# Kernel optimization log

Measured on AMD Instinct MI355X. Metric: run time of the kernel, lower is better.

## Reference

```python
import jax, jax.numpy as jnp
import numpy as np

N_NODES = 50000
N_EDGES = 800000
NUM_MOL = 2000
MSG_PASSES = 4


def setup_inputs() -> dict:
    key = jax.random.key(0)
    ks = jax.random.split(key, 16)
    x = jax.random.randint(ks[0], (N_NODES,), 0, 119)
    edge_attr = jax.random.randint(ks[1], (N_EDGES,), 0, 4)
    edge_index = jax.random.randint(ks[2], (2, N_EDGES), 0, N_NODES)
    batch = jnp.sort(jax.random.randint(ks[3], (N_NODES,), 0, NUM_MOL))
    f32 = jnp.float32
    return {
        "x": x,
        "edge_attr": edge_attr,
        "edge_index": edge_index,
        "batch": batch,
        "atom_table": jax.random.normal(ks[4], (119, 128), f32) * 0.1,
        "bond_table": jax.random.normal(ks[5], (4, 64), f32) * 0.1,
        "Wi": jax.random.normal(ks[6], (192, 128), f32) * 0.05,
        "bi": jax.random.normal(ks[7], (128,), f32) * 0.01,
        "Wu1": jax.random.normal(ks[8], (320, 128), f32) * 0.05,
        "bu1": jax.random.normal(ks[9], (128,), f32) * 0.01,
        "Wu2": jax.random.normal(ks[10], (128, 128), f32) * 0.05,
        "bu2": jax.random.normal(ks[11], (128,), f32) * 0.01,
        "Wr1": jax.random.normal(ks[12], (128, 512), f32) * 0.05,
        "br1": jax.random.normal(ks[13], (512,), f32) * 0.01,
        "Wr2": jax.random.normal(ks[14], (512, 1), f32) * 0.05,
        "br2": jax.random.normal(ks[15], (1,), f32) * 0.01,
    }


def reference(x, edge_attr, edge_index, batch,
              atom_table, bond_table, Wi, bi, Wu1, bu1, Wu2, bu2,
              Wr1, br1, Wr2, br2):
    atom = atom_table[x]                      # [N, atom_emb]
    bond = bond_table[edge_attr]              # [E, bond_emb]
    src, dst = edge_index[0], edge_index[1]
    a_src = atom[src]                         # [E, atom_emb]
    ab = jnp.concatenate([a_src, bond], axis=1)  # [E, atom_emb+bond_emb]
    msg = jax.nn.relu(ab @ Wi + bi)           # [E, msg_dim]
    for _ in range(MSG_PASSES):
        agg = jax.ops.segment_sum(msg, dst, num_segments=N_NODES)  # [N, msg_dim]
        upd_in = jnp.concatenate([ab, agg[src]], axis=1)           # [E, 320]
        h = jax.nn.relu(upd_in @ Wu1 + bu1)
        msg = jax.nn.relu(h @ Wu2 + bu2)
    node_state = jax.ops.segment_sum(msg, dst, num_segments=N_NODES)
    mol_state = jax.ops.segment_sum(node_state, batch, num_segments=NUM_MOL)
    out = jax.nn.relu(mol_state @ Wr1 + br1) @ Wr2 + br2  # [NUM_MOL, 1]
    return jnp.squeeze(out, axis=-1)
```

## Files before the change

### kernel.cpp

```cpp
#include <hip/hip_runtime.h>
#include <hip/hip_bf16.h>

#define N_NODES 50000
#define N_EDGES 800000
#define NUM_MOL 2000

typedef __attribute__((ext_vector_type(8))) short short8;
typedef __attribute__((ext_vector_type(4))) float f32x4;

union bfbits { __hip_bfloat16 b; short s; };

__global__ void k_tables(const float* __restrict__ atom_table,
                         const float* __restrict__ bond_table,
                         const float* __restrict__ Wi,
                         const float* __restrict__ bi,
                         const float* __restrict__ Wu1,
                         const float* __restrict__ bu1,
                         float* __restrict__ T1, float* __restrict__ U1,
                         float* __restrict__ T2c, float* __restrict__ U2c) {
  int b = blockIdx.x;
  int c = threadIdx.x;
  if (b < 119) {
    float t = 0.f, u = 0.f;
    for (int k = 0; k < 128; k++) {
      float a = atom_table[b * 128 + k];
      t += a * Wi[k * 128 + c];
      u += a * Wu1[k * 128 + c];
    }
    T1[b * 128 + c] = t;
    U1[b * 128 + c] = u;
  } else {
    int a = b - 119;
    float t = bi[c], u = bu1[c];
    for (int k = 0; k < 64; k++) {
      float bv = bond_table[a * 64 + k];
      t += bv * Wi[(128 + k) * 128 + c];
      u += bv * Wu1[(128 + k) * 128 + c];
    }
    T2c[a * 128 + c] = t;
    U2c[a * 128 + c] = u;
  }
}

__global__ void k_prep(const float* __restrict__ T1, const float* __restrict__ T2c,
                       const float* __restrict__ Wu2, const float* __restrict__ Wu1,
                       float* __restrict__ TT,
                       short* __restrict__ Wt, short* __restrict__ Wlo,
                       short* __restrict__ W1t, short* __restrict__ W1lo) {
  int b = blockIdx.x;
  int k = threadIdx.x;
  if (b < 476) {
    float v = T1[(b >> 2) * 128 + k] + T2c[(b & 3) * 128 + k];
    TT[b * 128 + k] = v > 0.f ? v : 0.f;
  } else if (b < 604) {
    int n = b - 476;
    float w = Wu2[k * 128 + n];
    bfbits hi; hi.b = __float2bfloat16(w);
    float hf = __bfloat162float(hi.b);
    bfbits lo; lo.b = __float2bfloat16(w - hf);
    Wt[n * 128 + k] = hi.s;
    Wlo[n * 128 + k] = lo.s;
  } else {
    int n = b - 604;
    float w = Wu1[(192 + k) * 128 + n];
    bfbits hi; hi.b = __float2bfloat16(w);
    float hf = __bfloat162float(hi.b);
    bfbits lo; lo.b = __float2bfloat16(w - hf);
    W1t[n * 128 + k] = hi.s;
    W1lo[n * 128 + k] = lo.s;
  }
}

__global__ void k_u1x(const int* __restrict__ x, const float* __restrict__ U1,
                      float* __restrict__ D_) {
  int n = blockIdx.x * 4 + (threadIdx.x >> 6);
  int lane = threadIdx.x & 63;
  int xn = x[n];
  float2 v = *(const float2*)&U1[xn * 128 + lane * 2];
  *(float2*)&D_[n * 128 + lane * 2] = v;
}

__global__ void k_fillb(const int* __restrict__ eidx, const int* __restrict__ attr,
                        const int* __restrict__ x,
                        int* __restrict__ cnt, int* __restrict__ csr1) {
  int e = blockIdx.x * 256 + threadIdx.x;
  int d = eidx[N_EDGES + e];
  int s = eidx[e];
  int a = attr[e];
  int pos = atomicAdd(&cnt[d], 1);
  if (pos < 64) {
    int packed = (s * 4 + a) | ((x[s] * 4 + a) << 18);
    csr1[d * 64 + pos] = packed;
  }
}

__global__ void k_molptr(const int* __restrict__ batch, int* __restrict__ molptr) {
  int m = blockIdx.x * 256 + threadIdx.x;
  if (m > NUM_MOL) return;
  int lo = 0, hi = N_NODES;
  while (lo < hi) {
    int mid = (lo + hi) >> 1;
    if (batch[mid] < m) lo = mid + 1; else hi = mid;
  }
  molptr[m] = lo;
}

__global__ void k_gather0(const int* __restrict__ cnt, const int* __restrict__ csr1,
                          const float* __restrict__ TT, float* __restrict__ A_) {
  int n = blockIdx.x * 4 + (threadIdx.x >> 6);
  int lane = threadIdx.x & 63;
  int g = lane >> 5;
  int p = lane & 31;
  int beg = n * 64;
  int end = beg + cnt[n];
  float s0 = 0.f, s1 = 0.f, s2 = 0.f, s3 = 0.f;
  int i = beg;
  for (; i + 7 < end; i += 8) {
    int iA = ((unsigned)csr1[i + g]) >> 18;
    int iB = ((unsigned)csr1[i + 2 + g]) >> 18;
    int iC = ((unsigned)csr1[i + 4 + g]) >> 18;
    int iD = ((unsigned)csr1[i + 6 + g]) >> 18;
    float4 va = *(const float4*)&TT[iA * 128 + p * 4];
    float4 vb = *(const float4*)&TT[iB * 128 + p * 4];
    float4 vc = *(const float4*)&TT[iC * 128 + p * 4];
    float4 vd = *(const float4*)&TT[iD * 128 + p * 4];
    s0 += (va.x + vb.x) + (vc.x + vd.x);
    s1 += (va.y + vb.y) + (vc.y + vd.y);
    s2 += (va.z + vb.z) + (vc.z + vd.z);
    s3 += (va.w + vb.w) + (vc.w + vd.w);
  }
  for (; i + 3 < end; i += 4) {
    int iA = ((unsigned)csr1[i + g]) >> 18;
    int iB = ((unsigned)csr1[i + 2 + g]) >> 18;
    float4 va = *(const float4*)&TT[iA * 128 + p * 4];
    float4 vb = *(const float4*)&TT[iB * 128 + p * 4];
    s0 += va.x + vb.x; s1 += va.y + vb.y;
    s2 += va.z + vb.z; s3 += va.w + vb.w;
  }
  for (; i < end; i += 2) {
    if (i + g < end) {
      int idx = ((unsigned)csr1[i + g]) >> 18;
      float4 v = *(const float4*)&TT[idx * 128 + p * 4];
      s0 += v.x; s1 += v.y; s2 += v.z; s3 += v.w;
    }
  }
  s0 += __shfl_xor(s0, 32, 64);
  s1 += __shfl_xor(s1, 32, 64);
  s2 += __shfl_xor(s2, 32, 64);
  s3 += __shfl_xor(s3, 32, 64);
  float2 o;
  o.x = (g == 0) ? s0 : s2;
  o.y = (g == 0) ? s1 : s3;
  *(float2*)&A_[n * 128 + p * 4 + g * 2] = o;
}

__global__ void k_gather(const int* __restrict__ cnt, const int* __restrict__ csr1,
                         const __hip_bfloat16* __restrict__ M, float* __restrict__ A_) {
  int n = blockIdx.x * 4 + (threadIdx.x >> 6);
  int lane = threadIdx.x & 63;
  int g = lane >> 4;
  int p = lane & 15;
  int beg = n * 64;
  int end = beg + cnt[n];
  float s[8];
#pragma unroll
  for (int j = 0; j < 8; j++) s[j] = 0.f;
  const short* Ms = (const short*)M;
  int i = beg;
  for (; i + 15 < end; i += 16) {
    int iA = csr1[i + g] & 0x3FFFF;
    int iB = csr1[i + 4 + g] & 0x3FFFF;
    int iC = csr1[i + 8 + g] & 0x3FFFF;
    int iD = csr1[i + 12 + g] & 0x3FFFF;
    short8 va = *(const short8*)&Ms[iA * 128 + p * 8];
    short8 vb = *(const short8*)&Ms[iB * 128 + p * 8];
    short8 vc = *(const short8*)&Ms[iC * 128 + p * 8];
    short8 vd = *(const short8*)&Ms[iD * 128 + p * 8];
#pragma unroll
    for (int j = 0; j < 4; j++) {
      float2 fa = __bfloat1622float2(*(const __hip_bfloat162*)&((const short*)&va)[j * 2]);
      float2 fb = __bfloat1622float2(*(const __hip_bfloat162*)&((const short*)&vb)[j * 2]);
      float2 fc = __bfloat1622float2(*(const __hip_bfloat162*)&((const short*)&vc)[j * 2]);
      float2 fd = __bfloat1622float2(*(const __hip_bfloat162*)&((const short*)&vd)[j * 2]);
      s[j * 2] += (fa.x + fb.x) + (fc.x + fd.x);
      s[j * 2 + 1] += (fa.y + fb.y) + (fc.y + fd.y);
    }
  }
  for (; i + 7 < end; i += 8) {
    int iA = csr1[i + g] & 0x3FFFF;
    int iB = csr1[i + 4 + g] & 0x3FFFF;
    short8 va = *(const short8*)&Ms[iA * 128 + p * 8];
    short8 vb = *(const short8*)&Ms[iB * 128 + p * 8];
#pragma unroll
    for (int j = 0; j < 4; j++) {
      float2 fa = __bfloat1622float2(*(const __hip_bfloat162*)&((const short*)&va)[j * 2]);
      float2 fb = __bfloat1622float2(*(const __hip_bfloat162*)&((const short*)&vb)[j * 2]);
      s[j * 2] += fa.x + fb.x;
      s[j * 2 + 1] += fa.y + fb.y;
    }
  }
  for (; i < end; i += 4) {
    if (i + g < end) {
      int idx = csr1[i + g] & 0x3FFFF;
      short8 va = *(const short8*)&Ms[idx * 128 + p * 8];
#pragma unroll
      for (int j = 0; j < 4; j++) {
        float2 fa = __bfloat1622float2(*(const __hip_bfloat162*)&((const short*)&va)[j * 2]);
        s[j * 2] += fa.x;
        s[j * 2 + 1] += fa.y;
      }
    }
  }
#pragma unroll
  for (int j = 0; j < 8; j++) s[j] += __shfl_xor(s[j], 16, 64);
#pragma unroll
  for (int j = 0; j < 8; j++) s[j] += __shfl_xor(s[j], 32, 64);
  float2 o;
  o.x = s[g * 2];
  o.y = s[g * 2 + 1];
  *(float2*)&A_[n * 128 + p * 8 + g * 2] = o;
}

__global__ __launch_bounds__(256, 2) void k_mm1m(const float* __restrict__ A_,
                                                 const short* __restrict__ W1t,
                                                 const short* __restrict__ W1lo,
                                                 const float* __restrict__ D_,
                                                 float* __restrict__ B2_) {
  __shared__ float mbuf[4][16][68];
  int t = threadIdx.x;
  int lane = t & 63;
  int m = lane & 15;
  int quad = lane >> 4;
  int wslot = t >> 6;
  int w0 = blockIdx.x * 4 + wslot;
  int h = w0 & 1;

  short8 whi[4][4], wlo[4][4];
#pragma unroll
  for (int kc = 0; kc < 4; kc++)
#pragma unroll
    for (int nt = 0; nt < 4; nt++) {
      int n = h * 64 + nt * 16 + m;
      whi[kc][nt] = *(const short8*)&W1t[n * 128 + kc * 32 + quad * 8];
      wlo[kc][nt] = *(const short8*)&W1lo[n * 128 + kc * 32 + quad * 8];
    }

  for (int tid = w0; tid < 6250; tid += 4096) {
    int s = tid >> 1;
    int row = s * 16 + m;
    f32x4 acc[4];
#pragma unroll
    for (int nt = 0; nt < 4; nt++) acc[nt] = (f32x4){0.f, 0.f, 0.f, 0.f};

#pragma unroll
    for (int kc = 0; kc < 4; kc++) {
      int k0 = kc * 32 + quad * 8;
      short8 ahi, alo;
      {
        float av[8];
        *(float4*)&av[0] = *(const float4*)&A_[row * 128 + k0];
        *(float4*)&av[4] = *(const float4*)&A_[row * 128 + k0 + 4];
#pragma unroll
        for (int j = 0; j < 8; j++) {
          float hv = av[j];
          bfbits hi; hi.b = __float2bfloat16(hv);
          float hf = __bfloat162float(hi.b);
          bfbits lo; lo.b = __float2bfloat16(hv - hf);
          ahi[j] = hi.s;
          alo[j] = lo.s;
        }
      }
#pragma unroll
      for (int nt = 0; nt < 4; nt++) {
        acc[nt] = __builtin_amdgcn_mfma_f32_16x16x32_bf16(ahi, whi[kc][nt], acc[nt], 0, 0, 0);
        acc[nt] = __builtin_amdgcn_mfma_f32_16x16x32_bf16(alo, whi[kc][nt], acc[nt], 0, 0, 0);
        acc[nt] = __builtin_amdgcn_mfma_f32_16x16x32_bf16(ahi, wlo[kc][nt], acc[nt], 0, 0, 0);
      }
    }

#pragma unroll
    for (int nt = 0; nt < 4; nt++)
#pragma unroll
      for (int r = 0; r < 4; r++)
        mbuf[wslot][quad * 4 + r][nt * 16 + m] = acc[nt][r];
#pragma unroll
    for (int p = 0; p < 4; p++) {
      int c = p * 64 + lane;
      int rr = c >> 4;
      int qf = c & 15;
      int n = s * 16 + rr;
      float4 v = *(const float4*)&mbuf[wslot][rr][qf * 4];
      float4 d = *(const float4*)&D_[n * 128 + h * 64 + qf * 4];
      v.x += d.x; v.y += d.y; v.z += d.z; v.w += d.w;
      *(float4*)&B2_[n * 128 + h * 64 + qf * 4] = v;
    }
  }
}

__global__ __launch_bounds__(256, 2) void k_mm2(const float* __restrict__ B2_,
                                                const float* __restrict__ U2c,
                                                const short* __restrict__ Wt,
                                                const short* __restrict__ Wlo,
                                                const float* __restrict__ bu2,
                                                __hip_bfloat16* __restrict__ M) {
  __shared__ short mbuf[4][16][68];
  int t = threadIdx.x;
  int lane = t & 63;
  int m = lane & 15;
  int quad = lane >> 4;
  int wslot = t >> 6;
  int w0 = blockIdx.x * 4 + wslot;
  int h = w0 & 1;

  short8 whi[4][4], wlo[4][4];
#pragma unroll
  for (int kc = 0; kc < 4; kc++)
#pragma unroll
    for (int nt = 0; nt < 4; nt++) {
      int n = h * 64 + nt * 16 + m;
      whi[kc][nt] = *(const short8*)&Wt[n * 128 + kc * 32 + quad * 8];
      wlo[kc][nt] = *(const short8*)&Wlo[n * 128 + kc * 32 + quad * 8];
    }
  float bias[4];
#pragma unroll
  for (int nt = 0; nt < 4; nt++) bias[nt] = bu2[h * 64 + nt * 16 + m];

  for (int tid = w0; tid < 25000; tid += 4096) {
    int s = tid >> 1;
    int node = s * 4 + (m >> 2);
    int attr = m & 3;
    f32x4 acc[4];
#pragma unroll
    for (int nt = 0; nt < 4; nt++) acc[nt] = (f32x4){0.f, 0.f, 0.f, 0.f};

#pragma unroll
    for (int kc = 0; kc < 4; kc++) {
      int k0 = kc * 32 + quad * 8;
      short8 ahi, alo;
      {
        float bba[8], u2a[8];
        *(float4*)&bba[0] = *(const float4*)&B2_[node * 128 + k0];
        *(float4*)&bba[4] = *(const float4*)&B2_[node * 128 + k0 + 4];
        *(float4*)&u2a[0] = *(const float4*)&U2c[attr * 128 + k0];
        *(float4*)&u2a[4] = *(const float4*)&U2c[attr * 128 + k0 + 4];
#pragma unroll
        for (int j = 0; j < 8; j++) {
          float hv = bba[j] + u2a[j];
          hv = hv > 0.f ? hv : 0.f;
          bfbits hi; hi.b = __float2bfloat16(hv);
          float hf = __bfloat162float(hi.b);
          bfbits lo; lo.b = __float2bfloat16(hv - hf);
          ahi[j] = hi.s;
          alo[j] = lo.s;
        }
      }
#pragma unroll
      for (int nt = 0; nt < 4; nt++) {
        acc[nt] = __builtin_amdgcn_mfma_f32_16x16x32_bf16(ahi, whi[kc][nt], acc[nt], 0, 0, 0);
        acc[nt] = __builtin_amdgcn_mfma_f32_16x16x32_bf16(alo, whi[kc][nt], acc[nt], 0, 0, 0);
        acc[nt] = __builtin_amdgcn_mfma_f32_16x16x32_bf16(ahi, wlo[kc][nt], acc[nt], 0, 0, 0);
      }
    }

#pragma unroll
    for (int nt = 0; nt < 4; nt++) {
#pragma unroll
      for (int r = 0; r < 4; r++) {
        float v = acc[nt][r] + bias[nt];
        v = v > 0.f ? v : 0.f;
        bfbits o; o.b = __float2bfloat16(v);
        mbuf[wslot][quad * 4 + r][nt * 16 + m] = o.s;
      }
    }
    {
      int rr = lane >> 2;
      int qq = lane & 3;
      short8 v = *(const short8*)&mbuf[wslot][rr][qq * 8];
      *(short8*)((short*)M + (s * 16 + rr) * 128 + h * 64 + qq * 8) = v;
      short8 v2 = *(const short8*)&mbuf[wslot][rr][(qq + 4) * 8];
      *(short8*)((short*)M + (s * 16 + rr) * 128 + h * 64 + (qq + 4) * 8) = v2;
    }
  }
}

__global__ void k_molgather(const float* __restrict__ A_, const int* __restrict__ molptr,
                            float* __restrict__ mol) {
  int m = blockIdx.x * 4 + (threadIdx.x >> 6);
  int lane = threadIdx.x & 63;
  int beg = molptr[m], end = molptr[m + 1];
  float ax = 0.f, ay = 0.f;
  int n = beg;
  for (; n + 1 < end; n += 2) {
    float2 v0 = *(const float2*)&A_[n * 128 + lane * 2];
    float2 v1 = *(const float2*)&A_[(n + 1) * 128 + lane * 2];
    ax += v0.x + v1.x;
    ay += v0.y + v1.y;
  }
  if (n < end) {
    float2 v0 = *(const float2*)&A_[n * 128 + lane * 2];
    ax += v0.x;
    ay += v0.y;
  }
  float2 o; o.x = ax; o.y = ay;
  *(float2*)&mol[m * 128 + lane * 2] = o;
}

__global__ __launch_bounds__(256) void k_readout(const float* __restrict__ mol,
                                                 const float* __restrict__ Wr1,
                                                 const float* __restrict__ br1,
                                                 const float* __restrict__ Wr2,
                                                 const float* __restrict__ br2,
                                                 float* __restrict__ out) {
  int m = blockIdx.x;
  __shared__ float ms[128];
  __shared__ float red[256];
  int t = threadIdx.x;
  if (t < 128) ms[t] = mol[m * 128 + t];
  __syncthreads();
  float part = 0.f;
#pragma unroll
  for (int jj = 0; jj < 2; jj++) {
    int j = t + jj * 256;
    float acc = br1[j];
#pragma unroll
    for (int k = 0; k < 128; k += 4) {
      float4 m4 = *(const float4*)&ms[k];
      acc += m4.x * Wr1[k * 512 + j] + m4.y * Wr1[(k + 1) * 512 + j] +
             m4.z * Wr1[(k + 2) * 512 + j] + m4.w * Wr1[(k + 3) * 512 + j];
    }
    acc = acc > 0.f ? acc : 0.f;
    part += acc * Wr2[j];
  }
  red[t] = part;
  __syncthreads();
  for (int s = 128; s > 0; s >>= 1) {
    if (t < s) red[t] += red[t + s];
    __syncthreads();
  }
  if (t == 0) out[m] = red[0] + br2[0];
}

extern "C" void kernel_launch(void* const* d_in, const int* in_sizes, int n_in,
                              void* d_out, int out_size, void* d_ws, size_t ws_size,
                              hipStream_t stream) {
  const int* x        = (const int*)d_in[0];
  const int* eattr    = (const int*)d_in[1];
  const int* eidx     = (const int*)d_in[2];
  const int* batch    = (const int*)d_in[3];
  const float* atom_table = (const float*)d_in[4];
  const float* bond_table = (const float*)d_in[5];
  const float* Wi  = (const float*)d_in[6];
  const float* bi  = (const float*)d_in[7];
  const float* Wu1 = (const float*)d_in[8];
  const float* bu1 = (const float*)d_in[9];
  const float* Wu2 = (const float*)d_in[10];
  const float* bu2 = (const float*)d_in[11];
  const float* Wr1 = (const float*)d_in[12];
  const float* br1 = (const float*)d_in[13];
  const float* Wr2 = (const float*)d_in[14];
  const float* br2 = (const float*)d_in[15];
  float* out = (float*)d_out;

  char* ws = (char*)d_ws;
  __hip_bfloat16* M = (__hip_bfloat16*)(ws);
  short* Wt      = (short*)(ws + 51200000);
  short* Wlo     = (short*)(ws + 51232768);
  short* W1t     = (short*)(ws + 51265536);
  short* W1lo    = (short*)(ws + 51298304);
  int*   molptr  = (int*)  (ws + 51331072);
  int*   cnt     = (int*)  (ws + 51340000);
  int*   csr1    = (int*)  (ws + 52000000);
  float* D       = (float*)(ws + 65000000);
  float* A       = (float*)(ws + 102400000);
  float* B2      = (float*)(ws + 128000000);
  float* T1      = (float*)(ws + 157000064);
  float* U1      = (float*)(ws + 157060992);
  float* T2c     = (float*)(ws + 157121920);
  float* U2c     = (float*)(ws + 157123968);
  float* TT      = (float*)(ws + 157126016);
  float* mol     = (float*)(ws + 157369728);

  hipMemsetAsync(cnt, 0, N_NODES * sizeof(int), stream);
  k_tables<<<123, 128, 0, stream>>>(atom_table, bond_table, Wi, bi, Wu1, bu1,
                                    T1, U1, T2c, U2c);
  k_prep<<<732, 128, 0, stream>>>(T1, T2c, Wu2, Wu1, TT, Wt, Wlo, W1t, W1lo);
  k_u1x<<<N_NODES / 4, 256, 0, stream>>>(x, U1, D);
  k_fillb<<<N_EDGES / 256, 256, 0, stream>>>(eidx, eattr, x, cnt, csr1);
  k_molptr<<<(NUM_MOL + 256) / 256, 256, 0, stream>>>(batch, molptr);

  k_gather0<<<N_NODES / 4, 256, 0, stream>>>(cnt, csr1, TT, A);

  for (int p = 0; p < 4; p++) {
    k_mm1m<<<1024, 256, 0, stream>>>(A, W1t, W1lo, D, B2);
    k_mm2<<<1024, 256, 0, stream>>>(B2, U2c, Wt, Wlo, bu2, M);
    k_gather<<<N_NODES / 4, 256, 0, stream>>>(cnt, csr1, M, A);
  }

  k_molgather<<<NUM_MOL / 4, 256, 0, stream>>>(A, molptr, mol);
  k_readout<<<NUM_MOL, 256, 0, stream>>>(mol, Wr1, br1, Wr2, br2, out);
}
```

Before: 633.6 us.

## Build CSR via two-pass destination binning instead of random global atomics

Replaces the single-pass CSR fill, which does random per-node atomics and scattered writes, with two passes. The first pass buckets edges into 256-node destination bins, split into 8 groups. The second pass, one block per bin, does the per-node atomics and writes within a localized region. The aim is better locality for atomics and CSR writes, at the cost of an extra kernel, an intermediate buffer in B2's workspace region, and a fixed bin capacity that silently drops edges if exceeded.

```diff
diff --git a/kernel.cpp b/kernel.cpp
--- a/kernel.cpp
+++ b/kernel.cpp
@@ -4,6 +4,9 @@
 #define N_NODES 50000
 #define N_EDGES 800000
 #define NUM_MOL 2000
+
+#define NBIN 196
+#define BINCAP 1536
 
 typedef __attribute__((ext_vector_type(8))) short short8;
 typedef __attribute__((ext_vector_type(4))) float f32x4;
@@ -80,17 +83,33 @@
   *(float2*)&D_[n * 128 + lane * 2] = v;
 }
 
-__global__ void k_fillb(const int* __restrict__ eidx, const int* __restrict__ attr,
-                        const int* __restrict__ x,
-                        int* __restrict__ cnt, int* __restrict__ csr1) {
+__global__ void k_bin(const int* __restrict__ eidx, const int* __restrict__ attr,
+                      const int* __restrict__ x,
+                      int* __restrict__ bincnt, int2* __restrict__ bins) {
   int e = blockIdx.x * 256 + threadIdx.x;
+  int grp = blockIdx.x & 7;
   int d = eidx[N_EDGES + e];
   int s = eidx[e];
   int a = attr[e];
-  int pos = atomicAdd(&cnt[d], 1);
-  if (pos < 64) {
+  int bin = d >> 8;
+  int pos = atomicAdd(&bincnt[grp * NBIN + bin], 1);
+  if (pos < BINCAP) {
     int packed = (s * 4 + a) | ((x[s] * 4 + a) << 18);
-    csr1[d * 64 + pos] = packed;
+    bins[(grp * NBIN + bin) * BINCAP + pos] = make_int2(packed, d);
+  }
+}
+
+__global__ void k_scatter(const int* __restrict__ bincnt, const int2* __restrict__ bins,
+                          int* __restrict__ cnt, int* __restrict__ csr1) {
+  int bin = blockIdx.x;
+  for (int grp = 0; grp < 8; grp++) {
+    int c = bincnt[grp * NBIN + bin];
+    if (c > BINCAP) c = BINCAP;
+    for (int i = threadIdx.x; i < c; i += 256) {
+      int2 r = bins[(grp * NBIN + bin) * BINCAP + i];
+      int pos = atomicAdd(&cnt[r.y], 1);
+      if (pos < 64) csr1[r.y * 64 + pos] = r.x;
+    }
   }
 }
 
@@ -480,12 +499,17 @@
   float* TT      = (float*)(ws + 157126016);
   float* mol     = (float*)(ws + 157369728);
 
+  int2* bins   = (int2*)(ws + 128000000);
+  int*  bincnt = (int*) (ws + 153600000);
+
   hipMemsetAsync(cnt, 0, N_NODES * sizeof(int), stream);
+  hipMemsetAsync(bincnt, 0, NBIN * 8 * sizeof(int), stream);
   k_tables<<<123, 128, 0, stream>>>(atom_table, bond_table, Wi, bi, Wu1, bu1,
                                     T1, U1, T2c, U2c);
   k_prep<<<732, 128, 0, stream>>>(T1, T2c, Wu2, Wu1, TT, Wt, Wlo, W1t, W1lo);
   k_u1x<<<N_NODES / 4, 256, 0, stream>>>(x, U1, D);
-  k_fillb<<<N_EDGES / 256, 256, 0, stream>>>(eidx, eattr, x, cnt, csr1);
+  k_bin<<<N_EDGES / 256, 256, 0, stream>>>(eidx, eattr, x, bincnt, bins);
+  k_scatter<<<NBIN, 256, 0, stream>>>(bincnt, bins, cnt, csr1);
   k_molptr<<<(NUM_MOL + 256) / 256, 256, 0, stream>>>(batch, molptr);
 
   k_gather0<<<N_NODES / 4, 256, 0, stream>>>(cnt, csr1, TT, A);
```

New measurement: 716.6 us. 1.13x slower.
